# Kernel tuning notes

Hardware: AMD Instinct MI355X
Metric: run time of the kernel (lower is better)

## Reference

```python
import jax, jax.numpy as jnp
import numpy as np

V, E, BLK, H = 32000, 1024, 2048, 16
D = E // H  # head size = 64


def setup_inputs() -> dict:
    key = jax.random.key(0)
    ks = jax.random.split(key, 10)
    s = 0.02
    idx = jax.random.randint(ks[0], (2, 2048), 0, V)
    targets = jax.random.randint(ks[1], (2, 2048), 0, V)
    tok_emb = jax.random.normal(ks[2], (V, E), jnp.float32) * s
    pos_emb = jax.random.normal(ks[3], (BLK, E), jnp.float32) * s
    wq = jax.random.normal(ks[4], (H, E, D), jnp.float32) * s
    wk = jax.random.normal(ks[5], (H, E, D), jnp.float32) * s
    wv = jax.random.normal(ks[6], (H, E, D), jnp.float32) * s
    w_ffn = jax.random.normal(ks[7], (E, E), jnp.float32) * s
    b_ffn = jnp.zeros((E,), jnp.float32)
    w_lm = jax.random.normal(ks[8], (E, V), jnp.float32) * s
    return dict(idx=idx, targets=targets, tok_emb=tok_emb, pos_emb=pos_emb,
                wq=wq, wk=wk, wv=wv, w_ffn=w_ffn, b_ffn=b_ffn, w_lm=w_lm)


def reference(idx, targets, tok_emb, pos_emb, wq, wk, wv, w_ffn, b_ffn, w_lm):
    B, T = idx.shape
    x = tok_emb[idx] + pos_emb[:T]              # [B,T,E]
    # per-head Q/K/V (all heads batched)
    q = jnp.einsum('bte,hed->bhtd', x, wq)
    k = jnp.einsum('bte,hed->bhtd', x, wk)
    v = jnp.einsum('bte,hed->bhtd', x, wv)
    # NOTE: original scales by C**-0.5 with C = n_embd (full dim), not head_size
    wei = jnp.einsum('bhtd,bhsd->bhts', q, k) * (E ** -0.5)
    causal = jnp.tril(jnp.ones((T, T), bool))
    wei = jnp.where(causal, wei, -jnp.inf)
    wei = jax.nn.softmax(wei, axis=-1)
    out = jnp.einsum('bhts,bhsd->bhtd', wei, v)  # [B,H,T,D]
    x = out.transpose(0, 2, 1, 3).reshape(B, T, E)  # concat heads
    x = jax.nn.relu(x @ w_ffn + b_ffn)           # FeedForward
    logits = x @ w_lm                            # [B,T,V]
    logp = jax.nn.log_softmax(logits, axis=-1)
    nll = -jnp.take_along_axis(logp, targets[..., None], axis=-1)[..., 0]
    loss = nll.mean()
    return logits, loss
```

## Files before the change

### kernel.cpp

```cpp
#include <hip/hip_runtime.h>

typedef unsigned short u16;
typedef __attribute__((ext_vector_type(4))) float floatx4;
typedef __attribute__((ext_vector_type(8))) short shortx8;

#define Bb 2
#define Tt 2048
#define Ee 1024
#define Hh 16
#define Dd 64
#define Vv 32000
#define Mm 4096

__device__ __forceinline__ u16 f2b(float x) {
  union { float f; unsigned u; } v; v.f = x;
  unsigned r = v.u + 0x7fffu + ((v.u >> 16) & 1u);
  return (u16)(r >> 16);
}

__device__ __forceinline__ void gload_lds16(const void* g, void* l) {
  __builtin_amdgcn_global_load_lds((__attribute__((address_space(1))) const void*)g,
                                   (__attribute__((address_space(3))) void*)l, 16, 0, 0);
}

__global__ __launch_bounds__(256) void embed_kernel(const int* __restrict__ idx,
                                                    const float* __restrict__ tok,
                                                    const float* __restrict__ pos,
                                                    u16* __restrict__ xout) {
  int i = blockIdx.x * 256 + threadIdx.x;
  int m = i >> 7, ch = i & 127;
  int t = m & (Tt - 1);
  int row = idx[m];
  const float4* ta = (const float4*)(tok + (size_t)row * Ee + ch * 8);
  const float4* pa = (const float4*)(pos + (size_t)t * Ee + ch * 8);
  float4 a0 = ta[0], a1 = ta[1], p0 = pa[0], p1 = pa[1];
  u16 r[8];
  r[0] = f2b(a0.x + p0.x); r[1] = f2b(a0.y + p0.y);
  r[2] = f2b(a0.z + p0.z); r[3] = f2b(a0.w + p0.w);
  r[4] = f2b(a1.x + p1.x); r[5] = f2b(a1.y + p1.y);
  r[6] = f2b(a1.z + p1.z); r[7] = f2b(a1.w + p1.w);
  *(uint4*)&xout[(size_t)m * Ee + ch * 8] = *(uint4*)r;
}

__global__ __launch_bounds__(256) void prep_qkv(const float* __restrict__ wq,
                                                const float* __restrict__ wk,
                                                const float* __restrict__ wv,
                                                u16* __restrict__ outT) {
  int o = blockIdx.x * 256 + threadIdx.x;
  int e = o & 1023, d = (o >> 10) & 63, h = (o >> 16) & 15, s = o >> 20;
  const float* w = (s == 0) ? wq : ((s == 1) ? wk : wv);
  outT[o] = f2b(w[((size_t)(h * Ee + e)) * Dd + d]);
}

__global__ __launch_bounds__(256) void transpose_f32_bf16(const float* __restrict__ in,
                                                          u16* __restrict__ out,
                                                          int R, int C) {
  __shared__ float tile[64][65];
  int c0 = blockIdx.x * 64, r0 = blockIdx.y * 64;
  int tid = threadIdx.x;
  for (int i = tid; i < 4096; i += 256) {
    int rr = i >> 6, cc = i & 63;
    tile[rr][cc] = in[(size_t)(r0 + rr) * C + c0 + cc];
  }
  __syncthreads();
  for (int i = tid; i < 4096; i += 256) {
    int cc = i >> 6, rr = i & 63;
    out[(size_t)(c0 + cc) * R + r0 + rr] = f2b(tile[rr][cc]);
  }
}

template <int EPI>
__global__ __launch_bounds__(256)
void gemm_bt(const u16* __restrict__ A, const u16* __restrict__ Bt,
             int M, int N, int K,
             float* __restrict__ Cf, u16* __restrict__ Cb,
             const float* __restrict__ bias,
             u16* __restrict__ q_out, u16* __restrict__ k_out, u16* __restrict__ v_out) {
  __shared__ u16 sA[128 * 32];
  __shared__ u16 sB[128 * 32];
  const int tid = threadIdx.x, lane = tid & 63, w = tid >> 6;
  const int quad = lane >> 4, l16 = lane & 15;
  const int m0 = blockIdx.y * 128, n0 = blockIdx.x * 128;
  const int wr = w >> 1, wc = w & 1;
  const int r4 = lane >> 2, c4 = lane & 3;

  floatx4 acc[4][4];
  floatx4 zz = {0.f, 0.f, 0.f, 0.f};
#pragma unroll
  for (int i = 0; i < 4; ++i)
#pragma unroll
    for (int j = 0; j < 4; ++j) acc[i][j] = zz;

  const int kiters = K >> 5;
  for (int kt = 0; kt < kiters; ++kt) {
    __syncthreads();
#pragma unroll
    for (int j = 0; j < 2; ++j) {
      const int rowblk = (w * 2 + j) * 16;
      gload_lds16(A + (size_t)(m0 + rowblk + r4) * K + (kt << 5) + c4 * 8, &sA[rowblk * 32]);
      gload_lds16(Bt + (size_t)(n0 + rowblk + r4) * K + (kt << 5) + c4 * 8, &sB[rowblk * 32]);
    }
    __syncthreads();
    shortx8 af[4], bfr[4];
#pragma unroll
    for (int mi = 0; mi < 4; ++mi)
      af[mi] = *(const shortx8*)&sA[(wr * 64 + mi * 16 + l16) * 32 + quad * 8];
#pragma unroll
    for (int ni = 0; ni < 4; ++ni)
      bfr[ni] = *(const shortx8*)&sB[(wc * 64 + ni * 16 + l16) * 32 + quad * 8];
#pragma unroll
    for (int mi = 0; mi < 4; ++mi)
#pragma unroll
      for (int ni = 0; ni < 4; ++ni)
        acc[mi][ni] = __builtin_amdgcn_mfma_f32_16x16x32_bf16(af[mi], bfr[ni], acc[mi][ni], 0, 0, 0);
  }

#pragma unroll
  for (int mi = 0; mi < 4; ++mi) {
#pragma unroll
    for (int r = 0; r < 4; ++r) {
      const int row = m0 + wr * 64 + mi * 16 + quad * 4 + r;
#pragma unroll
      for (int ni = 0; ni < 4; ++ni) {
        const int col = n0 + wc * 64 + ni * 16 + l16;
        float v = acc[mi][ni][r];
        if (EPI == 0) {
          Cf[(size_t)row * N + col] = v;
        } else if (EPI == 1) {
          v += bias[col];
          v = v > 0.f ? v : 0.f;
          Cb[(size_t)row * N + col] = f2b(v);
        } else {
          int s = col >> 10, hh = (col >> 6) & 15, d = col & 63;
          int b = row >> 11, t = row & (Tt - 1);
          if (s == 0)
            q_out[(((size_t)(b * Hh + hh)) * Tt + t) * Dd + d] = f2b(v * 0.03125f);
          else if (s == 1)
            k_out[(((size_t)(b * Hh + hh)) * Tt + t) * Dd + d] = f2b(v);
          else
            v_out[(((size_t)(b * Hh + hh)) * Dd + d) * Tt + t] = f2b(v);
        }
      }
    }
  }
}

__global__ __launch_bounds__(256) void attn_kernel(const u16* __restrict__ qg,
                                                   const u16* __restrict__ kg,
                                                   const u16* __restrict__ vg,
                                                   u16* __restrict__ outg) {
  const int qt = blockIdx.x, h = blockIdx.y, b = blockIdx.z;
  const int tid = threadIdx.x, lane = tid & 63, w = tid >> 6;
  const int quad = lane >> 4, l16 = lane & 15;
  __shared__ u16 sQ[64 * 64], sK[64 * 64], sV[64 * 64];
  __shared__ u16 sP[4][1024];
  const size_t bh = (size_t)b * Hh + h;
  const u16* qb = qg + bh * (Tt * Dd);
  const u16* kb = kg + bh * (Tt * Dd);
  const u16* vb = vg + bh * (Dd * Tt);
  const int q0 = qt * 64;

  for (int i = tid; i < 512; i += 256) {
    int row = i >> 3, ch = i & 7;
    *(uint4*)&sQ[row * 64 + ch * 8] = *(const uint4*)&qb[(size_t)(q0 + row) * Dd + ch * 8];
  }
  __syncthreads();
  shortx8 aq0 = *(const shortx8*)&sQ[(w * 16 + l16) * 64 + quad * 8];
  shortx8 aq1 = *(const shortx8*)&sQ[(w * 16 + l16) * 64 + 32 + quad * 8];

  floatx4 zz = {0.f, 0.f, 0.f, 0.f};
  floatx4 oacc[4];
  float mrow[4], lrow[4];
#pragma unroll
  for (int i = 0; i < 4; ++i) { oacc[i] = zz; mrow[i] = -__builtin_inff(); lrow[i] = 0.f; }

  for (int kt = 0; kt <= qt; ++kt) {
    const int k0 = kt * 64;
    __syncthreads();
    for (int i = tid; i < 512; i += 256) {
      int row = i >> 3, ch = i & 7;
      *(uint4*)&sK[row * 64 + ch * 8] = *(const uint4*)&kb[(size_t)(k0 + row) * Dd + ch * 8];
      *(uint4*)&sV[row * 64 + ch * 8] = *(const uint4*)&vb[(size_t)row * Tt + k0 + ch * 8];
    }
    __syncthreads();
    floatx4 s4[4] = {zz, zz, zz, zz};
#pragma unroll
    for (int ni = 0; ni < 4; ++ni) {
      shortx8 bk0 = *(const shortx8*)&sK[(ni * 16 + l16) * 64 + quad * 8];
      shortx8 bk1 = *(const shortx8*)&sK[(ni * 16 + l16) * 64 + 32 + quad * 8];
      s4[ni] = __builtin_amdgcn_mfma_f32_16x16x32_bf16(aq0, bk0, s4[ni], 0, 0, 0);
      s4[ni] = __builtin_amdgcn_mfma_f32_16x16x32_bf16(aq1, bk1, s4[ni], 0, 0, 0);
    }
    if (kt == qt) {
#pragma unroll
      for (int ni = 0; ni < 4; ++ni)
#pragma unroll
        for (int r = 0; r < 4; ++r) {
          int kloc = ni * 16 + l16, qloc = w * 16 + quad * 4 + r;
          if (kloc > qloc) s4[ni][r] = -__builtin_inff();
        }
    }
#pragma unroll
    for (int r = 0; r < 4; ++r) {
      float rm = fmaxf(fmaxf(s4[0][r], s4[1][r]), fmaxf(s4[2][r], s4[3][r]));
#pragma unroll
      for (int off = 8; off >= 1; off >>= 1) rm = fmaxf(rm, __shfl_xor(rm, off));
      float mnew = fmaxf(mrow[r], rm);
      float alpha = __expf(mrow[r] - mnew);
      float p[4], rsum = 0.f;
#pragma unroll
      for (int ni = 0; ni < 4; ++ni) { p[ni] = __expf(s4[ni][r] - mnew); rsum += p[ni]; }
#pragma unroll
      for (int off = 8; off >= 1; off >>= 1) rsum += __shfl_xor(rsum, off);
      lrow[r] = lrow[r] * alpha + rsum;
      mrow[r] = mnew;
#pragma unroll
      for (int di = 0; di < 4; ++di) oacc[di][r] *= alpha;
#pragma unroll
      for (int ni = 0; ni < 4; ++ni) sP[w][(quad * 4 + r) * 64 + ni * 16 + l16] = f2b(p[ni]);
    }
    __syncthreads();
    shortx8 ap0 = *(const shortx8*)&sP[w][l16 * 64 + quad * 8];
    shortx8 ap1 = *(const shortx8*)&sP[w][l16 * 64 + 32 + quad * 8];
#pragma unroll
    for (int di = 0; di < 4; ++di) {
      shortx8 bv0 = *(const shortx8*)&sV[(di * 16 + l16) * 64 + quad * 8];
      shortx8 bv1 = *(const shortx8*)&sV[(di * 16 + l16) * 64 + 32 + quad * 8];
      oacc[di] = __builtin_amdgcn_mfma_f32_16x16x32_bf16(ap0, bv0, oacc[di], 0, 0, 0);
      oacc[di] = __builtin_amdgcn_mfma_f32_16x16x32_bf16(ap1, bv1, oacc[di], 0, 0, 0);
    }
  }
#pragma unroll
  for (int di = 0; di < 4; ++di)
#pragma unroll
    for (int r = 0; r < 4; ++r) {
      int grow = b * Tt + q0 + w * 16 + quad * 4 + r;
      int col = h * Dd + di * 16 + l16;
      outg[(size_t)grow * Ee + col] = f2b(oacc[di][r] / lrow[r]);
    }
}

__global__ __launch_bounds__(256) void loss_row(const float* __restrict__ logits,
                                                const int* __restrict__ targets,
                                                float* __restrict__ nll) {
  const int m = blockIdx.x;
  const float* row = logits + (size_t)m * Vv;
  const int tid = threadIdx.x;
  float mx = -__builtin_inff(), sm = 0.f;
  for (int i = tid; i < Vv; i += 256) {
    float x = row[i];
    if (x > mx) { sm = sm * __expf(mx - x) + 1.f; mx = x; }
    else sm += __expf(x - mx);
  }
  __shared__ float red_m[256], red_s[256];
  red_m[tid] = mx; red_s[tid] = sm;
  __syncthreads();
  for (int s = 128; s > 0; s >>= 1) {
    if (tid < s) {
      float m1 = red_m[tid], s1 = red_s[tid];
      float m2 = red_m[tid + s], s2 = red_s[tid + s];
      float M = fmaxf(m1, m2);
      red_s[tid] = s1 * __expf(m1 - M) + s2 * __expf(m2 - M);
      red_m[tid] = M;
    }
    __syncthreads();
  }
  if (tid == 0) nll[m] = logf(red_s[0]) + red_m[0] - row[targets[m]];
}

__global__ __launch_bounds__(256) void loss_final(const float* __restrict__ nll,
                                                  float* __restrict__ out) {
  int tid = threadIdx.x;
  float s = 0.f;
  for (int i = tid; i < Mm; i += 256) s += nll[i];
  __shared__ float red[256];
  red[tid] = s;
  __syncthreads();
  for (int k = 128; k > 0; k >>= 1) {
    if (tid < k) red[tid] += red[tid + k];
    __syncthreads();
  }
  if (tid == 0) out[0] = red[0] * (1.f / (float)Mm);
}

extern "C" void kernel_launch(void* const* d_in, const int* in_sizes, int n_in,
                              void* d_out, int out_size, void* d_ws, size_t ws_size,
                              hipStream_t stream) {
  (void)in_sizes; (void)n_in; (void)out_size; (void)ws_size;
  const int* idx      = (const int*)d_in[0];
  const int* targets  = (const int*)d_in[1];
  const float* tok    = (const float*)d_in[2];
  const float* pos    = (const float*)d_in[3];
  const float* wq     = (const float*)d_in[4];
  const float* wk     = (const float*)d_in[5];
  const float* wv     = (const float*)d_in[6];
  const float* wffn   = (const float*)d_in[7];
  const float* bffn   = (const float*)d_in[8];
  const float* wlm    = (const float*)d_in[9];
  float* out = (float*)d_out;

  char* w8 = (char*)d_ws;
  u16* x_bf  = (u16*)(w8);
  u16* wqkvT = (u16*)(w8 + ((size_t)8 << 20));
  u16* qb    = (u16*)(w8 + ((size_t)14 << 20));
  u16* kb    = (u16*)(w8 + ((size_t)22 << 20));
  u16* vTb   = (u16*)(w8 + ((size_t)30 << 20));
  u16* attnb = (u16*)(w8 + ((size_t)38 << 20));
  u16* ffnb  = (u16*)(w8 + ((size_t)46 << 20));
  u16* wffnT = (u16*)(w8 + ((size_t)54 << 20));
  u16* wlmT  = (u16*)(w8 + ((size_t)56 << 20));
  float* nllp = (float*)(w8 + ((size_t)119 << 20));

  embed_kernel<<<2048, 256, 0, stream>>>(idx, tok, pos, x_bf);
  prep_qkv<<<(3 * Hh * Dd * Ee) / 256, 256, 0, stream>>>(wq, wk, wv, wqkvT);
  transpose_f32_bf16<<<dim3(Ee / 64, Ee / 64), 256, 0, stream>>>(wffn, wffnT, Ee, Ee);
  transpose_f32_bf16<<<dim3(Vv / 64, Ee / 64), 256, 0, stream>>>(wlm, wlmT, Ee, Vv);

  gemm_bt<2><<<dim3((3 * Hh * Dd) / 128, Mm / 128), 256, 0, stream>>>(
      x_bf, wqkvT, Mm, 3 * Hh * Dd, Ee, nullptr, nullptr, nullptr, qb, kb, vTb);

  attn_kernel<<<dim3(Tt / 64, Hh, Bb), 256, 0, stream>>>(qb, kb, vTb, attnb);

  gemm_bt<1><<<dim3(Ee / 128, Mm / 128), 256, 0, stream>>>(
      attnb, wffnT, Mm, Ee, Ee, nullptr, ffnb, bffn, nullptr, nullptr, nullptr);

  gemm_bt<0><<<dim3(Vv / 128, Mm / 128), 256, 0, stream>>>(
      ffnb, wlmT, Mm, Vv, Ee, out, nullptr, nullptr, nullptr, nullptr, nullptr);

  loss_row<<<Mm, 256, 0, stream>>>(out, targets, nllp);
  loss_final<<<1, 256, 0, stream>>>(nllp, out + (size_t)Mm * Vv);
}
```

Measured before the change: 1.461 ms.

## Fuse per-tile log-softmax statistics into LM-head GEMM epilogue and remap tiles

The LM-head GEMM epilogue now computes a per-row max and sum-of-exp for each 128-column tile and writes them to a stats buffer. The loss kernel then merges 250 partial stats per row instead of rereading the full 4096x32000 float logits matrix. This removes a large second pass over logits memory. GEMM workgroups are also remapped so that consecutive M-tiles land on the same XCD, and nontemporal loads and stores are used for weight transposition and the logits output. The cost is extra epilogue work in the GEMM and a stats buffer that reuses workspace already consumed by earlier stages.

```diff
diff --git a/kernel.cpp b/kernel.cpp
--- a/kernel.cpp
+++ b/kernel.cpp
@@ -11,6 +11,7 @@
 #define Dd 64
 #define Vv 32000
 #define Mm 4096
+#define NBLK_LM 250
 
 __device__ __forceinline__ u16 f2b(float x) {
   union { float f; unsigned u; } v; v.f = x;
@@ -60,7 +61,7 @@
   int tid = threadIdx.x;
   for (int i = tid; i < 4096; i += 256) {
     int rr = i >> 6, cc = i & 63;
-    tile[rr][cc] = in[(size_t)(r0 + rr) * C + c0 + cc];
+    tile[rr][cc] = __builtin_nontemporal_load(&in[(size_t)(r0 + rr) * C + c0 + cc]);
   }
   __syncthreads();
   for (int i = tid; i < 4096; i += 256) {
@@ -75,12 +76,16 @@
              int M, int N, int K,
              float* __restrict__ Cf, u16* __restrict__ Cb,
              const float* __restrict__ bias,
-             u16* __restrict__ q_out, u16* __restrict__ k_out, u16* __restrict__ v_out) {
+             u16* __restrict__ q_out, u16* __restrict__ k_out, u16* __restrict__ v_out,
+             float2* __restrict__ stats) {
   __shared__ u16 sA[128 * 32];
   __shared__ u16 sB[128 * 32];
   const int tid = threadIdx.x, lane = tid & 63, w = tid >> 6;
   const int quad = lane >> 4, l16 = lane & 15;
-  const int m0 = blockIdx.y * 128, n0 = blockIdx.x * 128;
+  const int wg = blockIdx.y * gridDim.x + blockIdx.x;
+  const int xcd = wg & 7, loc = wg >> 3;
+  const int bxs = loc >> 2, bys = (xcd << 2) + (loc & 3);
+  const int m0 = bys * 128, n0 = bxs * 128;
   const int wr = w >> 1, wc = w & 1;
   const int r4 = lane >> 2, c4 = lane & 3;
 
@@ -115,6 +120,46 @@
         acc[mi][ni] = __builtin_amdgcn_mfma_f32_16x16x32_bf16(af[mi], bfr[ni], acc[mi][ni], 0, 0, 0);
   }
 
+  if (EPI == 0) {
+    __syncthreads();
+    float* sm = (float*)sA;
+    float* ss = (float*)sB;
+#pragma unroll
+    for (int mi = 0; mi < 4; ++mi) {
+#pragma unroll
+      for (int r = 0; r < 4; ++r) {
+        const int rl = wr * 64 + mi * 16 + quad * 4 + r;
+        const int row = m0 + rl;
+        float v[4];
+#pragma unroll
+        for (int ni = 0; ni < 4; ++ni) {
+          v[ni] = acc[mi][ni][r];
+          const int col = n0 + wc * 64 + ni * 16 + l16;
+          __builtin_nontemporal_store(v[ni], &Cf[(size_t)row * N + col]);
+        }
+        float rmax = fmaxf(fmaxf(v[0], v[1]), fmaxf(v[2], v[3]));
+#pragma unroll
+        for (int off = 8; off >= 1; off >>= 1) rmax = fmaxf(rmax, __shfl_xor(rmax, off));
+        float se = __expf(v[0] - rmax) + __expf(v[1] - rmax) +
+                   __expf(v[2] - rmax) + __expf(v[3] - rmax);
+#pragma unroll
+        for (int off = 8; off >= 1; off >>= 1) se += __shfl_xor(se, off);
+        if (l16 == 0) { sm[rl * 2 + wc] = rmax; ss[rl * 2 + wc] = se; }
+      }
+    }
+    __syncthreads();
+    if (tid < 128) {
+      float m1 = sm[tid * 2], m2 = sm[tid * 2 + 1];
+      float s1 = ss[tid * 2], s2 = ss[tid * 2 + 1];
+      float Mx = fmaxf(m1, m2);
+      float2 st;
+      st.x = Mx;
+      st.y = s1 * __expf(m1 - Mx) + s2 * __expf(m2 - Mx);
+      stats[(size_t)bxs * M + m0 + tid] = st;
+    }
+    return;
+  }
+
 #pragma unroll
   for (int mi = 0; mi < 4; ++mi) {
 #pragma unroll
@@ -124,9 +169,7 @@
       for (int ni = 0; ni < 4; ++ni) {
         const int col = n0 + wc * 64 + ni * 16 + l16;
         float v = acc[mi][ni][r];
-        if (EPI == 0) {
-          Cf[(size_t)row * N + col] = v;
-        } else if (EPI == 1) {
+        if (EPI == 1) {
           v += bias[col];
           v = v > 0.f ? v : 0.f;
           Cb[(size_t)row * N + col] = f2b(v);
@@ -240,17 +283,16 @@
     }
 }
 
-__global__ __launch_bounds__(256) void loss_row(const float* __restrict__ logits,
-                                                const int* __restrict__ targets,
-                                                float* __restrict__ nll) {
+__global__ __launch_bounds__(256) void loss_row2(const float2* __restrict__ stats,
+                                                 const float* __restrict__ logits,
+                                                 const int* __restrict__ targets,
+                                                 float* __restrict__ nll) {
   const int m = blockIdx.x;
-  const float* row = logits + (size_t)m * Vv;
   const int tid = threadIdx.x;
   float mx = -__builtin_inff(), sm = 0.f;
-  for (int i = tid; i < Vv; i += 256) {
-    float x = row[i];
-    if (x > mx) { sm = sm * __expf(mx - x) + 1.f; mx = x; }
-    else sm += __expf(x - mx);
+  if (tid < NBLK_LM) {
+    float2 p = stats[(size_t)tid * Mm + m];
+    mx = p.x; sm = p.y;
   }
   __shared__ float red_m[256], red_s[256];
   red_m[tid] = mx; red_s[tid] = sm;
@@ -265,7 +307,8 @@
     }
     __syncthreads();
   }
-  if (tid == 0) nll[m] = logf(red_s[0]) + red_m[0] - row[targets[m]];
+  if (tid == 0)
+    nll[m] = logf(red_s[0]) + red_m[0] - logits[(size_t)m * Vv + targets[m]];
 }
 
 __global__ __launch_bounds__(256) void loss_final(const float* __restrict__ nll,
@@ -310,6 +353,7 @@
   u16* wffnT = (u16*)(w8 + ((size_t)54 << 20));
   u16* wlmT  = (u16*)(w8 + ((size_t)56 << 20));
   float* nllp = (float*)(w8 + ((size_t)119 << 20));
+  float2* stats = (float2*)(w8);
 
   embed_kernel<<<2048, 256, 0, stream>>>(idx, tok, pos, x_bf);
   prep_qkv<<<(3 * Hh * Dd * Ee) / 256, 256, 0, stream>>>(wq, wk, wv, wqkvT);
@@ -317,16 +361,16 @@
   transpose_f32_bf16<<<dim3(Vv / 64, Ee / 64), 256, 0, stream>>>(wlm, wlmT, Ee, Vv);
 
   gemm_bt<2><<<dim3((3 * Hh * Dd) / 128, Mm / 128), 256, 0, stream>>>(
-      x_bf, wqkvT, Mm, 3 * Hh * Dd, Ee, nullptr, nullptr, nullptr, qb, kb, vTb);
+      x_bf, wqkvT, Mm, 3 * Hh * Dd, Ee, nullptr, nullptr, nullptr, qb, kb, vTb, nullptr);
 
   attn_kernel<<<dim3(Tt / 64, Hh, Bb), 256, 0, stream>>>(qb, kb, vTb, attnb);
 
   gemm_bt<1><<<dim3(Ee / 128, Mm / 128), 256, 0, stream>>>(
-      attnb, wffnT, Mm, Ee, Ee, nullptr, ffnb, bffn, nullptr, nullptr, nullptr);
+      attnb, wffnT, Mm, Ee, Ee, nullptr, ffnb, bffn, nullptr, nullptr, nullptr, nullptr);
 
   gemm_bt<0><<<dim3(Vv / 128, Mm / 128), 256, 0, stream>>>(
-      ffnb, wlmT, Mm, Vv, Ee, out, nullptr, nullptr, nullptr, nullptr, nullptr);
-
-  loss_row<<<Mm, 256, 0, stream>>>(out, targets, nllp);
+      ffnb, wlmT, Mm, Vv, Ee, out, nullptr, nullptr, nullptr, nullptr, nullptr, stats);
+
+  loss_row2<<<Mm, 256, 0, stream>>>(stats, out, targets, nllp);
   loss_final<<<1, 256, 0, stream>>>(nllp, out + (size_t)Mm * Vv);
 }
```

New measurement: 1.241 ms. 1.18x faster.
